# Optimization experiments

Measured on AMD Instinct MI355X. Metric: run time of the kernel, lower is better.

Reference implementation:

```python
import jax, jax.numpy as jnp
import numpy as np


def _conv2d(x, w):
    # x: [N, C, H, W], w: [O, I, kh, kw], stride 1, SAME padding
    return jax.lax.conv_general_dilated(
        x, w, window_strides=(1, 1), padding='SAME',
        dimension_numbers=('NCHW', 'OIHW', 'NCHW'))


def setup_inputs() -> dict:
    key = jax.random.key(0)
    k0, k1, k2 = jax.random.split(key, 3)
    T, B, C, H, W, HID = 16, 4, 32, 64, 64, 64
    x = jax.random.normal(k0, (T, B, C, H, W), dtype=jnp.float32)
    # ConvLSTM params: x2h conv (in->4*hid), h2h conv (hid->4*hid)
    w_x2h = jax.random.normal(k1, (4 * HID, C, 3, 3), dtype=jnp.float32) * 0.05
    b_x2h = jnp.zeros((4 * HID,), dtype=jnp.float32)
    w_h2h = jax.random.normal(k2, (4 * HID, HID, 3, 3), dtype=jnp.float32) * 0.05
    b_h2h = jnp.zeros((4 * HID,), dtype=jnp.float32)
    return {'x': x, 'w_x2h': w_x2h, 'b_x2h': b_x2h, 'w_h2h': w_h2h, 'b_h2h': b_h2h}


def reference(x, w_x2h, b_x2h, w_h2h, b_h2h):
    # x: [T, B, C, H, W]
    T, B, C, H, W = x.shape
    HID = w_h2h.shape[1]
    # x2h applied time-distributed (the nn.Module's x2h(x) before the time loop)
    xg = _conv2d(x.reshape(T * B, C, H, W), w_x2h) + b_x2h[:, None, None]
    xg = xg.reshape(T, B, 4 * HID, H, W)

    h0 = jnp.zeros((B, HID, H, W), dtype=x.dtype)
    c0 = jnp.zeros((B, HID, H, W), dtype=x.dtype)

    def step(carry, xt):
        h, c = carry
        gates = xt + _conv2d(h, w_h2h) + b_h2h[:, None, None]  # [B, 4*HID, H, W]
        i, f, g, o = jnp.split(gates, 4, axis=1)
        i = jax.nn.sigmoid(i)
        f = jax.nn.sigmoid(f)
        o = jax.nn.sigmoid(o)
        g = jnp.tanh(g)
        c = f * c + i * g
        h = o * jnp.tanh(c)
        return (h, c), h

    _, hs = jax.lax.scan(step, (h0, c0), xg)  # hs: [T, B, HID, H, W]
    return hs
```

## Files before the change

kernel.cpp:

```cpp
#include <hip/hip_runtime.h>


#define TSTEPS 16
#define BATCH  4
#define CX     32
#define HID    64
#define HW     64
#define PW     66
#define QS     528
#define XROW   2112
#define HROW   4224
#define LROW   1088
#define SROWS  6

typedef _Float16 f16x8 __attribute__((ext_vector_type(8)));
typedef float f32x4  __attribute__((ext_vector_type(4)));
typedef unsigned short u16x4 __attribute__((ext_vector_type(4)));

__device__ __forceinline__ float sigmoidf_(float x){ return 1.0f/(1.0f+__expf(-x)); }
__device__ __forceinline__ float tanhf_(float x){ return 1.0f - 2.0f/(__expf(2.0f*x)+1.0f); }

__device__ __forceinline__ unsigned short f2h(float f){
  return __builtin_bit_cast(unsigned short, (_Float16)f);
}

__device__ __forceinline__ void gload_lds16(const void* g, void* l){
  __builtin_amdgcn_global_load_lds(
      (const __attribute__((address_space(1))) void*)g,
      (__attribute__((address_space(3))) void*)l, 16, 0, 0);
}


__global__ __launch_bounds__(256) void prep_w(
    const float* __restrict__ wx, const float* __restrict__ wh,
    unsigned short* __restrict__ wxT, unsigned short* __restrict__ whT)
{
  int idx = blockIdx.x*256 + threadIdx.x;
  if (idx < 9*256*64){
    int tap = idx / (256*64);
    int rem = idx - tap*(256*64);
    int o = rem >> 6, c = rem & 63;
    int g = o >> 6, chunk = (o >> 4) & 3, h16 = o & 15;
    int kc = c >> 5, cc = c & 31, q = cc >> 3, c8 = cc & 7;
    whT[(size_t)(tap*4 + chunk)*4096 + kc*2048 + (g*64 + q*16 + h16)*8 + c8] =
        f2h(wh[(o*HID + c)*9 + tap]);
  }
  if (idx < 9*256*32){
    int tap = idx / (256*32);
    int rem = idx - tap*(256*32);
    int o = rem >> 5, c = rem & 31;
    int g = o >> 6, chunk = (o >> 4) & 3, h16 = o & 15;
    int q = c >> 3, c8 = c & 7;
    wxT[(size_t)(tap*4 + chunk)*2048 + (g*64 + q*16 + h16)*8 + c8] =
        f2h(wx[(o*CX + c)*9 + tap]);
  }
}

__global__ __launch_bounds__(256) void prep_x(
    const float* __restrict__ x, unsigned short* __restrict__ xT)
{
  __shared__ float tile[CX][HW];
  const int tb = blockIdx.x, yp = blockIdx.y, tid = threadIdx.x;
  const int y = yp - 1;
  const bool rowok = (y >= 0 && y < HW);
  if (rowok){
    const float* src = x + (size_t)tb*CX*HW*HW + y*HW;
    for (int i = tid; i < CX*HW; i += 256){
      int c = i >> 6, xc = i & 63;
      tile[c][xc] = src[(size_t)c*HW*HW + xc];
    }
  }
  __syncthreads();
  size_t base = ((size_t)tb*PW + yp)*XROW;
  for (int i = tid; i < PW*CX; i += 256){
    int xp = i >> 5, c = i & 31;
    int xg = xp - 1;
    float v = (rowok && xg >= 0 && xg < HW) ? tile[c][xg] : 0.f;
    xT[base + ((size_t)(c >> 3)*PW + xp)*8 + (c & 7)] = f2h(v);
  }
}

__global__ __launch_bounds__(256) void zero_ws(unsigned long long* p, size_t n64){
  size_t i = (size_t)blockIdx.x*256 + threadIdx.x;
  size_t stride = (size_t)gridDim.x*256;
  for (; i < n64; i += stride) p[i] = 0ull;
}


#define MFMA(a,b,c) __builtin_amdgcn_mfma_f32_16x16x32_f16((a),(b),(c),0,0,0)

template<int FIRST>
__global__ __launch_bounds__(512, 4) void step_mfma(
    const unsigned short* __restrict__ xT,
    const unsigned short* __restrict__ wxT, const unsigned short* __restrict__ whT,
    const unsigned short* __restrict__ hp, unsigned short* __restrict__ hc,
    const float* __restrict__ bxb, const float* __restrict__ bhb,
    float* __restrict__ c_state,
    float* __restrict__ h_out,
    int t)
{
  __shared__ __attribute__((aligned(16))) short xs[SROWS*LROW];
  __shared__ __attribute__((aligned(16))) short hs[2*SROWS*LROW];

  const int tid  = threadIdx.x;
  const int lane = tid & 63;
  const int w    = tid >> 6;
  const int chl  = w >> 2;
  const int wy   = w & 3;
  const int nn = lane & 15, q = lane >> 4;
  const int cp = blockIdx.x >> 1, xh = blockIdx.x & 1;
  const int chunk = cp*2 + chl;
  const int y0 = blockIdx.y * 4;
  const int b  = blockIdx.z;
  const int m0 = chunk * 16;
  const int y  = y0 + wy;
  const int tb = t*BATCH + b;
  const int wfo = (q*16 + nn)*8;

  const size_t cslot =
      (((size_t)((blockIdx.z*16 + blockIdx.y)*4 + blockIdx.x))*512 + tid)*8;

  {
    const size_t xbase = ((size_t)tb*PW + y0)*XROW;
    int px = tid % 34, j = tid / 34;
#pragma unroll 1
    for (int i = tid; i < SROWS*4*34; i += 512){
      const int qq = j & 3;
      const int r  = j >> 2;
      const unsigned short* src = xT
          + xbase + (size_t)r*XROW + qq*QS + (xh*32 + px)*8;
      gload_lds16(src, &xs[(size_t)i*8]);
      px += 2; j += 15; if (px >= 34){ px -= 34; ++j; }
    }
  }
  if (!FIRST){
    const size_t hbase = ((size_t)b*PW + y0)*HROW;
    int px = tid % 34, j = tid / 34;
#pragma unroll 1
    for (int i = tid; i < SROWS*8*34; i += 512){
      const int kcq = j & 7;
      const int r   = j >> 3;
      const unsigned short* src = hp
          + hbase + (size_t)r*HROW + kcq*QS + (xh*32 + px)*8;
      gload_lds16(src, &hs[(size_t)i*8]);
      px += 2; j += 15; if (px >= 34){ px -= 34; ++j; }
    }
  }

  f32x4 cpre[2];
  if (!FIRST){
    cpre[0] = *(const f32x4*)&c_state[cslot];
    cpre[1] = *(const f32x4*)&c_state[cslot + 4];
  } else {
    cpre[0] = (f32x4){0.f,0.f,0.f,0.f};
    cpre[1] = (f32x4){0.f,0.f,0.f,0.f};
  }

  f32x4 acc[4][2];
#pragma unroll
  for (int g = 0; g < 4; ++g)
#pragma unroll
    for (int ns = 0; ns < 2; ++ns)
      acc[g][ns] = (f32x4){0.f, 0.f, 0.f, 0.f};

  __syncthreads();

#pragma unroll
  for (int tap = 0; tap < 9; ++tap){
    const int ky = tap / 3;
    const int kx = tap - ky*3;
    const int r0 = wy + ky;
    const int ps = kx + nn;

    {
      const unsigned short* wp = wxT + (size_t)(tap*4 + chunk)*2048 + wfo;
      f16x8 ax[4];
#pragma unroll
      for (int g = 0; g < 4; ++g) ax[g] = *(const f16x8*)(wp + g*512);
      f16x8 bxf[2];
#pragma unroll
      for (int ns = 0; ns < 2; ++ns)
        bxf[ns] = *(const f16x8*)&xs[r0*LROW + (q*34 + ns*16 + ps)*8];
      __builtin_amdgcn_s_setprio(1);
#pragma unroll
      for (int ns = 0; ns < 2; ++ns)
#pragma unroll
        for (int g = 0; g < 4; ++g)
          acc[g][ns] = MFMA(ax[g], bxf[ns], acc[g][ns]);
      __builtin_amdgcn_s_setprio(0);
    }

    if (!FIRST){
      const unsigned short* hpw = whT + (size_t)(tap*4 + chunk)*4096 + wfo;
      f16x8 ah[2][4];
#pragma unroll
      for (int kc = 0; kc < 2; ++kc)
#pragma unroll
        for (int g = 0; g < 4; ++g) ah[kc][g] = *(const f16x8*)(hpw + kc*2048 + g*512);
      f16x8 bhf[2][2];
#pragma unroll
      for (int kc = 0; kc < 2; ++kc)
#pragma unroll
        for (int ns = 0; ns < 2; ++ns)
          bhf[kc][ns] = *(const f16x8*)&hs[(r0*2 + kc)*LROW + (q*34 + ns*16 + ps)*8];
      __builtin_amdgcn_s_setprio(1);
#pragma unroll
      for (int kc = 0; kc < 2; ++kc)
#pragma unroll
        for (int ns = 0; ns < 2; ++ns)
#pragma unroll
          for (int g = 0; g < 4; ++g)
            acc[g][ns] = MFMA(ah[kc][g], bhf[kc][ns], acc[g][ns]);
      __builtin_amdgcn_s_setprio(0);
    }
  }

  f32x4 bv[4];
#pragma unroll
  for (int g = 0; g < 4; ++g){
    f32x4 ba = *(const f32x4*)&bxb[g*HID + m0 + 4*q];
    f32x4 bb = *(const f32x4*)&bhb[g*HID + m0 + 4*q];
    bv[g] = ba + bb;
  }
  const int kcE = chunk >> 1;
  const int qhE = ((chunk & 1) << 1) | (q >> 1);
  const int c8b = (q & 1) * 4;
#pragma unroll
  for (int ns = 0; ns < 2; ++ns){
    const int xg = xh*32 + ns*16 + nn;
    f32x4 cn;
    float hn[4];
#pragma unroll
    for (int r = 0; r < 4; ++r){
      float iv = sigmoidf_(acc[0][ns][r] + bv[0][r]);
      float fv = sigmoidf_(acc[1][ns][r] + bv[1][r]);
      float gv = tanhf_  (acc[2][ns][r] + bv[2][r]);
      float ov = sigmoidf_(acc[3][ns][r] + bv[3][r]);
      float cnv = fv*cpre[ns][r] + iv*gv;
      cn[r] = cnv;
      hn[r] = ov * tanhf_(cnv);
    }
    *(f32x4*)&c_state[cslot + ns*4] = cn;
#pragma unroll
    for (int r = 0; r < 4; ++r)
      h_out[(((size_t)b*HID + m0 + 4*q + r)*HW + y)*HW + xg] = hn[r];
    const size_t hoff = ((size_t)b*PW + (y+1))*HROW + (kcE*4 + qhE)*QS + (xg+1)*8 + c8b;
    u16x4 ph;
#pragma unroll
    for (int r = 0; r < 4; ++r) ph[r] = f2h(hn[r]);
    *(u16x4*)&hc[hoff] = ph;
  }
}


#define FCHUNK  8
#define FTILE_H 16
#define FROWS   (FTILE_H + 2)
#define FSTRIDE 68

__device__ __forceinline__ void do_chunk_f(
    float tile[FCHUNK][FROWS][FSTRIDE],
    const float* __restrict__ src,
    const float* __restrict__ wp0, const float* __restrict__ wp1,
    const float* __restrict__ wp2, const float* __restrict__ wp3,
    int gy0, int txg, int ty, int tid, float (&acc)[4][2][4])
{
  __syncthreads();
  for (int s = tid; s < FCHUNK * FROWS * 32; s += 128) {
    int c2 = s & 31;
    int rowid = s >> 5;
    int ic = rowid / FROWS;
    int r  = rowid - ic * FROWS;
    int gy = gy0 - 1 + r;
    if ((unsigned)gy < (unsigned)HW) {
      float2 v = *(const float2*)&src[(ic << 12) + (gy << 6) + (c2 << 1)];
      *(float2*)&tile[ic][r][2 + (c2 << 1)] = v;
    }
  }
  __syncthreads();
  for (int ic = 0; ic < FCHUNK; ++ic) {
    float w0[9], w1[9], w2[9], w3[9];
#pragma unroll
    for (int k = 0; k < 9; ++k) {
      w0[k] = wp0[ic*9+k]; w1[k] = wp1[ic*9+k];
      w2[k] = wp2[ic*9+k]; w3[k] = wp3[ic*9+k];
    }
    float rv[4][8];
#pragma unroll
    for (int rr = 0; rr < 4; ++rr) {
      const float* p = &tile[ic][2*ty+rr][4*txg];
      float4 a  = *(const float4*)p;
      float4 bb = *(const float4*)(p + 4);
      rv[rr][0]=a.x; rv[rr][1]=a.y; rv[rr][2]=a.z; rv[rr][3]=a.w;
      rv[rr][4]=bb.x; rv[rr][5]=bb.y; rv[rr][6]=bb.z; rv[rr][7]=bb.w;
    }
#pragma unroll
    for (int j = 0; j < 2; ++j)
#pragma unroll
      for (int dy = 0; dy < 3; ++dy)
#pragma unroll
        for (int qq = 0; qq < 4; ++qq)
#pragma unroll
          for (int dx = 0; dx < 3; ++dx) {
            float v = rv[j+dy][qq+dx+1];
            int k = dy*3+dx;
            acc[0][j][qq] = fmaf(v, w0[k], acc[0][j][qq]);
            acc[1][j][qq] = fmaf(v, w1[k], acc[1][j][qq]);
            acc[2][j][qq] = fmaf(v, w2[k], acc[2][j][qq]);
            acc[3][j][qq] = fmaf(v, w3[k], acc[3][j][qq]);
          }
  }
}

__global__ __launch_bounds__(128) void convlstm_step_f(
    const float* __restrict__ x_t, const float* __restrict__ h_prev,
    const float* __restrict__ w_x2h, const float* __restrict__ b_x2h,
    const float* __restrict__ w_h2h, const float* __restrict__ b_h2h,
    float* __restrict__ c_state, float* __restrict__ h_out, int first)
{
  __shared__ float tile[FCHUNK][FROWS][FSTRIDE];
  const int txg = threadIdx.x, ty = threadIdx.y;
  const int tid = ty*16 + txg;
  const int by = blockIdx.x, hc = blockIdx.y, b = blockIdx.z;
  const int gy0 = by * FTILE_H;
  {
    float2* p = (float2*)&tile[0][0][0];
    for (int i = tid; i < FCHUNK*FROWS*FSTRIDE/2; i += 128)
      p[i] = make_float2(0.f, 0.f);
  }
  float acc[4][2][4];
#pragma unroll
  for (int g = 0; g < 4; ++g)
#pragma unroll
    for (int j = 0; j < 2; ++j)
#pragma unroll
      for (int qq = 0; qq < 4; ++qq) acc[g][j][qq] = 0.f;
  {
    const float* wx0 = w_x2h + (size_t)(0*HID+hc)*CX*9;
    const float* wx1 = w_x2h + (size_t)(1*HID+hc)*CX*9;
    const float* wx2 = w_x2h + (size_t)(2*HID+hc)*CX*9;
    const float* wx3 = w_x2h + (size_t)(3*HID+hc)*CX*9;
    for (int c0 = 0; c0 < CX; c0 += FCHUNK)
      do_chunk_f(tile, x_t + ((size_t)(b*CX+c0) << 12),
                 wx0+c0*9, wx1+c0*9, wx2+c0*9, wx3+c0*9, gy0, txg, ty, tid, acc);
  }
  if (!first){
    const float* wh0 = w_h2h + (size_t)(0*HID+hc)*HID*9;
    const float* wh1 = w_h2h + (size_t)(1*HID+hc)*HID*9;
    const float* wh2 = w_h2h + (size_t)(2*HID+hc)*HID*9;
    const float* wh3 = w_h2h + (size_t)(3*HID+hc)*HID*9;
    for (int c0 = 0; c0 < HID; c0 += FCHUNK)
      do_chunk_f(tile, h_prev + ((size_t)(b*HID+c0) << 12),
                 wh0+c0*9, wh1+c0*9, wh2+c0*9, wh3+c0*9, gy0, txg, ty, tid, acc);
  }
  const float bi = b_x2h[0*HID+hc] + b_h2h[0*HID+hc];
  const float bf = b_x2h[1*HID+hc] + b_h2h[1*HID+hc];
  const float bg = b_x2h[2*HID+hc] + b_h2h[2*HID+hc];
  const float bo = b_x2h[3*HID+hc] + b_h2h[3*HID+hc];
#pragma unroll
  for (int j = 0; j < 2; ++j){
    const int row = gy0 + 2*ty + j;
    const int off = ((b*HID + hc)*HW + row)*HW + 4*txg;
    float4 cpv4 = make_float4(0.f,0.f,0.f,0.f);
    if (!first) cpv4 = *(const float4*)&c_state[off];
    float cn[4], hn[4];
    const float cpv[4] = {cpv4.x, cpv4.y, cpv4.z, cpv4.w};
#pragma unroll
    for (int qq = 0; qq < 4; ++qq){
      const float ig = sigmoidf_(acc[0][j][qq] + bi);
      const float fg = sigmoidf_(acc[1][j][qq] + bf);
      const float gg = tanhf_  (acc[2][j][qq] + bg);
      const float og = sigmoidf_(acc[3][j][qq] + bo);
      const float cnv = fg*cpv[qq] + ig*gg;
      cn[qq] = cnv;
      hn[qq] = og * tanhf_(cnv);
    }
    *(float4*)&c_state[off] = make_float4(cn[0],cn[1],cn[2],cn[3]);
    *(float4*)&h_out[off]   = make_float4(hn[0],hn[1],hn[2],hn[3]);
  }
}


extern "C" void kernel_launch(void* const* d_in, const int* in_sizes, int n_in,
                              void* d_out, int out_size, void* d_ws, size_t ws_size,
                              hipStream_t stream) {
  const float* x     = (const float*)d_in[0];
  const float* w_x2h = (const float*)d_in[1];
  const float* b_x2h = (const float*)d_in[2];
  const float* w_h2h = (const float*)d_in[3];
  const float* b_h2h = (const float*)d_in[4];
  float* out = (float*)d_out;

  size_t off = 0;
  auto alloc = [&](size_t bytes) -> char* {
    char* p = (char*)d_ws + off;
    off += (bytes + 255) & ~(size_t)255;
    return p;
  };
  float* c_state = (float*)alloc((size_t)256*512*8*4);
  unsigned short* wxT = (unsigned short*)alloc((size_t)9*4*2048*2);
  unsigned short* whT = (unsigned short*)alloc((size_t)9*4*4096*2);
  const size_t hT_bytes = (size_t)BATCH*PW*HROW*2;
  unsigned short* hA = (unsigned short*)alloc(hT_bytes);
  unsigned short* hB = (unsigned short*)alloc(hT_bytes);
  const size_t xT_bytes = (size_t)TSTEPS*BATCH*PW*XROW*2;
  unsigned short* xT = (unsigned short*)alloc(xT_bytes);
  const size_t need = off;

  const size_t x_step = (size_t)BATCH*CX*HW*HW;
  const size_t h_step = (size_t)BATCH*HID*HW*HW;

  if (need <= ws_size) {
    prep_w<<<(9*256*HID + 255)/256, 256, 0, stream>>>(w_x2h, w_h2h, wxT, whT);
    prep_x<<<dim3(TSTEPS*BATCH, PW), 256, 0, stream>>>(x, xT);
    zero_ws<<<1024, 256, 0, stream>>>((unsigned long long*)hA, 2*hT_bytes/8);

    for (int t = 0; t < TSTEPS; ++t) {
      unsigned short* hp = (t & 1) ? hA : hB;
      unsigned short* hc = (t & 1) ? hB : hA;
      if (t == 0)
        step_mfma<1><<<dim3(4, 16, BATCH), 512, 0, stream>>>(
            xT, wxT, whT, hp, hc, b_x2h, b_h2h,
            c_state, out + (size_t)t*h_step, t);
      else
        step_mfma<0><<<dim3(4, 16, BATCH), 512, 0, stream>>>(
            xT, wxT, whT, hp, hc, b_x2h, b_h2h,
            c_state, out + (size_t)t*h_step, t);
    }
  } else {
    dim3 grid(HW / FTILE_H, HID, BATCH);
    dim3 block(16, 8);
    for (int t = 0; t < TSTEPS; ++t) {
      const float* x_t    = x + (size_t)t*x_step;
      const float* h_prev = (t == 0) ? x : out + (size_t)(t-1)*h_step;
      float* h_out        = out + (size_t)t*h_step;
      convlstm_step_f<<<grid, block, 0, stream>>>(
          x_t, h_prev, w_x2h, b_x2h, w_h2h, b_h2h, c_state, h_out, t == 0 ? 1 : 0);
    }
  }
}
```

Measured before the change: 326.2 us.

## Merge prep kernels into one launch, prefetch tap-0 weights, relax launch bounds

The three preprocessing kernels (weight transpose, input padding/transpose, hidden-buffer zeroing) are merged into a single launch, with a block-index switch choosing each role. This removes two kernel launches and their gaps. In the step kernel, the tap-0 weight fragments are loaded into registers before the barrier so their global latency overlaps the LDS staging. The launch bounds minimum-blocks hint drops from 4 to 2, which allows more registers per thread but may lower occupancy.

```diff
diff --git a/kernel.cpp b/kernel.cpp
--- a/kernel.cpp
+++ b/kernel.cpp
@@ -13,6 +13,10 @@
 #define LROW   1088
 #define SROWS  6
 
+#define PXBLK  4224
+#define PWBLK  576
+#define PZBLK  1024
+
 typedef _Float16 f16x8 __attribute__((ext_vector_type(8)));
 typedef float f32x4  __attribute__((ext_vector_type(4)));
 typedef unsigned short u16x4 __attribute__((ext_vector_type(4)));
@@ -30,67 +34,67 @@
       (__attribute__((address_space(3))) void*)l, 16, 0, 0);
 }
 
-
-__global__ __launch_bounds__(256) void prep_w(
+__global__ __launch_bounds__(256) void prep_all(
+    const float* __restrict__ x,
     const float* __restrict__ wx, const float* __restrict__ wh,
-    unsigned short* __restrict__ wxT, unsigned short* __restrict__ whT)
-{
-  int idx = blockIdx.x*256 + threadIdx.x;
-  if (idx < 9*256*64){
-    int tap = idx / (256*64);
-    int rem = idx - tap*(256*64);
-    int o = rem >> 6, c = rem & 63;
-    int g = o >> 6, chunk = (o >> 4) & 3, h16 = o & 15;
-    int kc = c >> 5, cc = c & 31, q = cc >> 3, c8 = cc & 7;
-    whT[(size_t)(tap*4 + chunk)*4096 + kc*2048 + (g*64 + q*16 + h16)*8 + c8] =
-        f2h(wh[(o*HID + c)*9 + tap]);
-  }
-  if (idx < 9*256*32){
-    int tap = idx / (256*32);
-    int rem = idx - tap*(256*32);
-    int o = rem >> 5, c = rem & 31;
-    int g = o >> 6, chunk = (o >> 4) & 3, h16 = o & 15;
-    int q = c >> 3, c8 = c & 7;
-    wxT[(size_t)(tap*4 + chunk)*2048 + (g*64 + q*16 + h16)*8 + c8] =
-        f2h(wx[(o*CX + c)*9 + tap]);
-  }
-}
-
-__global__ __launch_bounds__(256) void prep_x(
-    const float* __restrict__ x, unsigned short* __restrict__ xT)
+    unsigned short* __restrict__ xT,
+    unsigned short* __restrict__ wxT, unsigned short* __restrict__ whT,
+    unsigned long long* __restrict__ hz, size_t hz64)
 {
   __shared__ float tile[CX][HW];
-  const int tb = blockIdx.x, yp = blockIdx.y, tid = threadIdx.x;
-  const int y = yp - 1;
-  const bool rowok = (y >= 0 && y < HW);
-  if (rowok){
-    const float* src = x + (size_t)tb*CX*HW*HW + y*HW;
-    for (int i = tid; i < CX*HW; i += 256){
-      int c = i >> 6, xc = i & 63;
-      tile[c][xc] = src[(size_t)c*HW*HW + xc];
-    }
-  }
-  __syncthreads();
-  size_t base = ((size_t)tb*PW + yp)*XROW;
-  for (int i = tid; i < PW*CX; i += 256){
-    int xp = i >> 5, c = i & 31;
-    int xg = xp - 1;
-    float v = (rowok && xg >= 0 && xg < HW) ? tile[c][xg] : 0.f;
-    xT[base + ((size_t)(c >> 3)*PW + xp)*8 + (c & 7)] = f2h(v);
-  }
-}
-
-__global__ __launch_bounds__(256) void zero_ws(unsigned long long* p, size_t n64){
-  size_t i = (size_t)blockIdx.x*256 + threadIdx.x;
-  size_t stride = (size_t)gridDim.x*256;
-  for (; i < n64; i += stride) p[i] = 0ull;
+  const int bid = blockIdx.x, tid = threadIdx.x;
+
+  if (bid < PXBLK){
+    const int tb = bid / 66, yp = bid - tb*66;
+    const int y = yp - 1;
+    const bool rowok = (y >= 0 && y < HW);
+    if (rowok){
+      const float* src = x + (size_t)tb*CX*HW*HW + y*HW;
+      for (int i = tid; i < CX*HW; i += 256){
+        int c = i >> 6, xc = i & 63;
+        tile[c][xc] = src[(size_t)c*HW*HW + xc];
+      }
+    }
+    __syncthreads();
+    size_t base = ((size_t)tb*PW + yp)*XROW;
+    for (int i = tid; i < PW*CX; i += 256){
+      int xp = i >> 5, c = i & 31;
+      int xg = xp - 1;
+      float v = (rowok && xg >= 0 && xg < HW) ? tile[c][xg] : 0.f;
+      xT[base + ((size_t)(c >> 3)*PW + xp)*8 + (c & 7)] = f2h(v);
+    }
+  } else if (bid < PXBLK + PWBLK){
+    int idx = (bid - PXBLK)*256 + tid;
+    if (idx < 9*256*64){
+      int tap = idx / (256*64);
+      int rem = idx - tap*(256*64);
+      int o = rem >> 6, c = rem & 63;
+      int g = o >> 6, chunk = (o >> 4) & 3, h16 = o & 15;
+      int kc = c >> 5, cc = c & 31, q = cc >> 3, c8 = cc & 7;
+      whT[(size_t)(tap*4 + chunk)*4096 + kc*2048 + (g*64 + q*16 + h16)*8 + c8] =
+          f2h(wh[(o*HID + c)*9 + tap]);
+    }
+    if (idx < 9*256*32){
+      int tap = idx / (256*32);
+      int rem = idx - tap*(256*32);
+      int o = rem >> 5, c = rem & 31;
+      int g = o >> 6, chunk = (o >> 4) & 3, h16 = o & 15;
+      int q = c >> 3, c8 = c & 7;
+      wxT[(size_t)(tap*4 + chunk)*2048 + (g*64 + q*16 + h16)*8 + c8] =
+          f2h(wx[(o*CX + c)*9 + tap]);
+    }
+  } else {
+    size_t i = (size_t)(bid - PXBLK - PWBLK)*256 + tid;
+    const size_t stride = (size_t)PZBLK*256;
+    for (; i < hz64; i += stride) hz[i] = 0ull;
+  }
 }
 
 
 #define MFMA(a,b,c) __builtin_amdgcn_mfma_f32_16x16x32_f16((a),(b),(c),0,0,0)
 
 template<int FIRST>
-__global__ __launch_bounds__(512, 4) void step_mfma(
+__global__ __launch_bounds__(512, 2) void step_mfma(
     const unsigned short* __restrict__ xT,
     const unsigned short* __restrict__ wxT, const unsigned short* __restrict__ whT,
     const unsigned short* __restrict__ hp, unsigned short* __restrict__ hc,
@@ -156,6 +160,21 @@
     cpre[1] = (f32x4){0.f,0.f,0.f,0.f};
   }
 
+  f16x8 ax0[4];
+  f16x8 ah0[2][4];
+  {
+    const unsigned short* wp0 = wxT + (size_t)chunk*2048 + wfo;
+#pragma unroll
+    for (int g = 0; g < 4; ++g) ax0[g] = *(const f16x8*)(wp0 + g*512);
+    if (!FIRST){
+      const unsigned short* hp0 = whT + (size_t)chunk*4096 + wfo;
+#pragma unroll
+      for (int kc = 0; kc < 2; ++kc)
+#pragma unroll
+        for (int g = 0; g < 4; ++g) ah0[kc][g] = *(const f16x8*)(hp0 + kc*2048 + g*512);
+    }
+  }
+
   f32x4 acc[4][2];
 #pragma unroll
   for (int g = 0; g < 4; ++g)
@@ -173,10 +192,15 @@
     const int ps = kx + nn;
 
     {
-      const unsigned short* wp = wxT + (size_t)(tap*4 + chunk)*2048 + wfo;
       f16x8 ax[4];
-#pragma unroll
-      for (int g = 0; g < 4; ++g) ax[g] = *(const f16x8*)(wp + g*512);
+      if (tap == 0){
+#pragma unroll
+        for (int g = 0; g < 4; ++g) ax[g] = ax0[g];
+      } else {
+        const unsigned short* wp = wxT + (size_t)(tap*4 + chunk)*2048 + wfo;
+#pragma unroll
+        for (int g = 0; g < 4; ++g) ax[g] = *(const f16x8*)(wp + g*512);
+      }
       f16x8 bxf[2];
 #pragma unroll
       for (int ns = 0; ns < 2; ++ns)
@@ -191,12 +215,19 @@
     }
 
     if (!FIRST){
-      const unsigned short* hpw = whT + (size_t)(tap*4 + chunk)*4096 + wfo;
       f16x8 ah[2][4];
-#pragma unroll
-      for (int kc = 0; kc < 2; ++kc)
-#pragma unroll
-        for (int g = 0; g < 4; ++g) ah[kc][g] = *(const f16x8*)(hpw + kc*2048 + g*512);
+      if (tap == 0){
+#pragma unroll
+        for (int kc = 0; kc < 2; ++kc)
+#pragma unroll
+          for (int g = 0; g < 4; ++g) ah[kc][g] = ah0[kc][g];
+      } else {
+        const unsigned short* hpw = whT + (size_t)(tap*4 + chunk)*4096 + wfo;
+#pragma unroll
+        for (int kc = 0; kc < 2; ++kc)
+#pragma unroll
+          for (int g = 0; g < 4; ++g) ah[kc][g] = *(const f16x8*)(hpw + kc*2048 + g*512);
+      }
       f16x8 bhf[2][2];
 #pragma unroll
       for (int kc = 0; kc < 2; ++kc)
@@ -411,9 +442,9 @@
   const size_t h_step = (size_t)BATCH*HID*HW*HW;
 
   if (need <= ws_size) {
-    prep_w<<<(9*256*HID + 255)/256, 256, 0, stream>>>(w_x2h, w_h2h, wxT, whT);
-    prep_x<<<dim3(TSTEPS*BATCH, PW), 256, 0, stream>>>(x, xT);
-    zero_ws<<<1024, 256, 0, stream>>>((unsigned long long*)hA, 2*hT_bytes/8);
+    prep_all<<<PXBLK + PWBLK + PZBLK, 256, 0, stream>>>(
+        x, w_x2h, w_h2h, xT, wxT, whT,
+        (unsigned long long*)hA, 2*hT_bytes/8);
 
     for (int t = 0; t < TSTEPS; ++t) {
       unsigned short* hp = (t & 1) ? hA : hB;
```

Measured after the change: 330.6 us. About the same (+1.3%).
